# Kernel tuning notes

Hardware: AMD Instinct MI355X
Metric: run time of the kernel (lower is better)

Reference implementation:

```python
import jax, jax.numpy as jnp
import numpy as np

KY, KX = 3, 3  # kernel_size from init_kwargs


def setup_inputs() -> dict:
    key = jax.random.key(0)
    x = jax.random.normal(key, (8, 64, 256, 256), dtype=jnp.float32)
    return {"x": x}


def reference(x):
    # NMS: mask = x > max over 3x3 replicate-padded neighborhood EXCLUDING center.
    # Note: the torch conv kernel zeroes the center row, so the center output
    # channel is all zeros and the max implicitly includes 0 — we replicate that
    # by initializing the running max to zeros.
    ky, kx = KY, KX
    py, px = (ky - 1) // 2, (kx - 1) // 2
    H, W = x.shape[-2], x.shape[-1]
    xp = jnp.pad(x, ((0, 0), (0, 0), (py, py), (px, px)), mode='edge')  # replicate pad
    numel = ky * kx
    center = numel // 2
    max_non_center = jnp.zeros_like(x)  # zeroed-center channel participates in max
    for i in range(numel):  # fixed small kernel window, unrolled (8 shifts)
        if i == center:
            continue
        dy, dx = divmod(i, kx)
        max_non_center = jnp.maximum(max_non_center, xp[..., dy:dy + H, dx:dx + W])
    mask = x > max_non_center
    return x * mask.astype(x.dtype)
```

## Files before the change

### kernel.cpp

```cpp
#include <hip/hip_runtime.h>


#define NMS_H 256
#define NMS_W 256
#define ROWS_PER_THREAD 16

struct Row6 {
    float l, v0, v1, v2, v3, r;
};

__device__ __forceinline__ Row6 load_row6(const float* __restrict__ plane, int row, int col4) {
    const float4 v = *reinterpret_cast<const float4*>(plane + row * NMS_W + col4);
    Row6 r6;
    r6.v0 = v.x; r6.v1 = v.y; r6.v2 = v.z; r6.v3 = v.w;
    r6.l = (col4 == 0)              ? v.x : plane[row * NMS_W + col4 - 1];
    r6.r = (col4 + 4 >= NMS_W)      ? v.w : plane[row * NMS_W + col4 + 4];
    return r6;
}

__global__ __launch_bounds__(256) void nms2d_kernel(const float* __restrict__ x,
                                                    float* __restrict__ out) {
    const int plane_idx = blockIdx.x >> 2;
    const int strip     = blockIdx.x & 3;
    const int col4      = threadIdx.x * 4;
    const int r0        = strip * 64 + threadIdx.y * ROWS_PER_THREAD;

    const float* plane  = x   + (size_t)plane_idx * (NMS_H * NMS_W);
    float*       oplane = out + (size_t)plane_idx * (NMS_H * NMS_W);

    Row6 rm = load_row6(plane, max(r0 - 1, 0), col4);
    Row6 rc = load_row6(plane, r0, col4);

    #pragma unroll
    for (int i = 0; i < ROWS_PER_THREAD; ++i) {
        const int r = r0 + i;
        Row6 rp = load_row6(plane, min(r + 1, NMS_H - 1), col4);

        float4 o;
        {
            float m = fmaxf(0.0f, fmaxf(rm.l, fmaxf(rm.v0, rm.v1)));
            m = fmaxf(m, fmaxf(rc.l, rc.v1));
            m = fmaxf(m, fmaxf(rp.l, fmaxf(rp.v0, rp.v1)));
            o.x = (rc.v0 > m) ? rc.v0 : 0.0f;
        }
        {
            float m = fmaxf(0.0f, fmaxf(rm.v0, fmaxf(rm.v1, rm.v2)));
            m = fmaxf(m, fmaxf(rc.v0, rc.v2));
            m = fmaxf(m, fmaxf(rp.v0, fmaxf(rp.v1, rp.v2)));
            o.y = (rc.v1 > m) ? rc.v1 : 0.0f;
        }
        {
            float m = fmaxf(0.0f, fmaxf(rm.v1, fmaxf(rm.v2, rm.v3)));
            m = fmaxf(m, fmaxf(rc.v1, rc.v3));
            m = fmaxf(m, fmaxf(rp.v1, fmaxf(rp.v2, rp.v3)));
            o.z = (rc.v2 > m) ? rc.v2 : 0.0f;
        }
        {
            float m = fmaxf(0.0f, fmaxf(rm.v2, fmaxf(rm.v3, rm.r)));
            m = fmaxf(m, fmaxf(rc.v2, rc.r));
            m = fmaxf(m, fmaxf(rp.v2, fmaxf(rp.v3, rp.r)));
            o.w = (rc.v3 > m) ? rc.v3 : 0.0f;
        }

        *reinterpret_cast<float4*>(oplane + r * NMS_W + col4) = o;

        rm = rc;
        rc = rp;
    }
}

extern "C" void kernel_launch(void* const* d_in, const int* in_sizes, int n_in,
                              void* d_out, int out_size, void* d_ws, size_t ws_size,
                              hipStream_t stream) {
    const float* x = (const float*)d_in[0];
    float* out = (float*)d_out;

    dim3 block(64, 4);
    dim3 grid(512 * 4);
    nms2d_kernel<<<grid, block, 0, stream>>>(x, out);
}
```

Baseline: 235.2 us.

## Use wavefront shuffles for halo columns, preload rows, reuse row maxima, nontemporal stores

Horizontal neighbours now come from cross-lane shuffles within the 64-wide wavefront instead of extra scalar global loads. Each thread loads all ten rows it needs up front and computes per-row horizontal maxima once, reusing them across three output rows. Output uses nontemporal stores, and rows per thread drop to 8 with twice as many blocks. Halo-row reloads per thread rise relative to the rows it outputs, and register use goes up from the preloaded rows.

```diff
diff --git a/kernel.cpp b/kernel.cpp
--- a/kernel.cpp
+++ b/kernel.cpp
@@ -3,69 +3,68 @@
 
 #define NMS_H 256
 #define NMS_W 256
-#define ROWS_PER_THREAD 16
+#define ROWS 8
 
-struct Row6 {
-    float l, v0, v1, v2, v3, r;
+typedef float f4_t __attribute__((ext_vector_type(4)));
+
+struct RowMax {
+    float4 h;
+    float4 lr;
 };
 
-__device__ __forceinline__ Row6 load_row6(const float* __restrict__ plane, int row, int col4) {
-    const float4 v = *reinterpret_cast<const float4*>(plane + row * NMS_W + col4);
-    Row6 r6;
-    r6.v0 = v.x; r6.v1 = v.y; r6.v2 = v.z; r6.v3 = v.w;
-    r6.l = (col4 == 0)              ? v.x : plane[row * NMS_W + col4 - 1];
-    r6.r = (col4 + 4 >= NMS_W)      ? v.w : plane[row * NMS_W + col4 + 4];
-    return r6;
+__device__ __forceinline__ RowMax rowmax(const float4 v, const int tx) {
+    float l = __shfl_up(v.w, 1, 64);
+    float r = __shfl_down(v.x, 1, 64);
+    if (tx == 0)  l = v.x;
+    if (tx == 63) r = v.w;
+    RowMax o;
+    o.h.x = fmaxf(l,   fmaxf(v.x, v.y));
+    o.h.y = fmaxf(v.x, fmaxf(v.y, v.z));
+    o.h.z = fmaxf(v.y, fmaxf(v.z, v.w));
+    o.h.w = fmaxf(v.z, fmaxf(v.w, r));
+    o.lr.x = fmaxf(l,   v.y);
+    o.lr.y = fmaxf(v.x, v.z);
+    o.lr.z = fmaxf(v.y, v.w);
+    o.lr.w = fmaxf(v.z, r);
+    return o;
 }
 
 __global__ __launch_bounds__(256) void nms2d_kernel(const float* __restrict__ x,
                                                     float* __restrict__ out) {
-    const int plane_idx = blockIdx.x >> 2;
-    const int strip     = blockIdx.x & 3;
-    const int col4      = threadIdx.x * 4;
-    const int r0        = strip * 64 + threadIdx.y * ROWS_PER_THREAD;
+    const int plane_idx = blockIdx.x >> 3;
+    const int strip     = blockIdx.x & 7;
+    const int tx        = threadIdx.x;
+    const int col4      = tx * 4;
+    const int r0        = strip * (ROWS * 4) + threadIdx.y * ROWS;
 
     const float* plane  = x   + (size_t)plane_idx * (NMS_H * NMS_W);
     float*       oplane = out + (size_t)plane_idx * (NMS_H * NMS_W);
 
-    Row6 rm = load_row6(plane, max(r0 - 1, 0), col4);
-    Row6 rc = load_row6(plane, r0, col4);
+    float4 v[ROWS + 2];
+    #pragma unroll
+    for (int i = 0; i < ROWS + 2; ++i) {
+        const int r = min(max(r0 + i - 1, 0), NMS_H - 1);
+        v[i] = *reinterpret_cast<const float4*>(plane + r * NMS_W + col4);
+    }
+
+    RowMax a = rowmax(v[0], tx);
+    RowMax b = rowmax(v[1], tx);
 
     #pragma unroll
-    for (int i = 0; i < ROWS_PER_THREAD; ++i) {
-        const int r = r0 + i;
-        Row6 rp = load_row6(plane, min(r + 1, NMS_H - 1), col4);
+    for (int i = 0; i < ROWS; ++i) {
+        RowMax c = rowmax(v[i + 2], tx);
+        const float4 ctr = v[i + 1];
+        float4 o;
+        float m;
+        m = fmaxf(0.0f, fmaxf(fmaxf(a.h.x, c.h.x), b.lr.x)); o.x = (ctr.x > m) ? ctr.x : 0.0f;
+        m = fmaxf(0.0f, fmaxf(fmaxf(a.h.y, c.h.y), b.lr.y)); o.y = (ctr.y > m) ? ctr.y : 0.0f;
+        m = fmaxf(0.0f, fmaxf(fmaxf(a.h.z, c.h.z), b.lr.z)); o.z = (ctr.z > m) ? ctr.z : 0.0f;
+        m = fmaxf(0.0f, fmaxf(fmaxf(a.h.w, c.h.w), b.lr.w)); o.w = (ctr.w > m) ? ctr.w : 0.0f;
 
-        float4 o;
-        {
-            float m = fmaxf(0.0f, fmaxf(rm.l, fmaxf(rm.v0, rm.v1)));
-            m = fmaxf(m, fmaxf(rc.l, rc.v1));
-            m = fmaxf(m, fmaxf(rp.l, fmaxf(rp.v0, rp.v1)));
-            o.x = (rc.v0 > m) ? rc.v0 : 0.0f;
-        }
-        {
-            float m = fmaxf(0.0f, fmaxf(rm.v0, fmaxf(rm.v1, rm.v2)));
-            m = fmaxf(m, fmaxf(rc.v0, rc.v2));
-            m = fmaxf(m, fmaxf(rp.v0, fmaxf(rp.v1, rp.v2)));
-            o.y = (rc.v1 > m) ? rc.v1 : 0.0f;
-        }
-        {
-            float m = fmaxf(0.0f, fmaxf(rm.v1, fmaxf(rm.v2, rm.v3)));
-            m = fmaxf(m, fmaxf(rc.v1, rc.v3));
-            m = fmaxf(m, fmaxf(rp.v1, fmaxf(rp.v2, rp.v3)));
-            o.z = (rc.v2 > m) ? rc.v2 : 0.0f;
-        }
-        {
-            float m = fmaxf(0.0f, fmaxf(rm.v2, fmaxf(rm.v3, rm.r)));
-            m = fmaxf(m, fmaxf(rc.v2, rc.r));
-            m = fmaxf(m, fmaxf(rp.v2, fmaxf(rp.v3, rp.r)));
-            o.w = (rc.v3 > m) ? rc.v3 : 0.0f;
-        }
+        f4_t ov = {o.x, o.y, o.z, o.w};
+        __builtin_nontemporal_store(ov, reinterpret_cast<f4_t*>(oplane + (r0 + i) * NMS_W + col4));
 
-        *reinterpret_cast<float4*>(oplane + r * NMS_W + col4) = o;
-
-        rm = rc;
-        rc = rp;
+        a = b; b = c;
     }
 }
 
@@ -76,6 +75,6 @@
     float* out = (float*)d_out;
 
     dim3 block(64, 4);
-    dim3 grid(512 * 4);
+    dim3 grid(512 * 8);
     nms2d_kernel<<<grid, block, 0, stream>>>(x, out);
 }
```

After: 230.2 us. 2.1% less time.
